# Kernel optimization log

Measured on AMD Instinct MI355X. Metric: run time of the kernel, lower is better.

## Reference

```python
import jax, jax.numpy as jnp
import numpy as np

B, N, NFEAT, NHID, NOUT, NMLP, NCLASS = 32, 1024, 128, 64, 64, 128, 2
ALPHA = 0.2  # leaky relu slope
NEG = -9e15


def setup_inputs() -> dict:
    key = jax.random.key(0)
    ks = jax.random.split(key, 12)
    x = jax.random.normal(ks[0], (B, N, NFEAT), dtype=jnp.float32)
    x_mask = (jax.random.uniform(ks[1], (B, N)) < 0.9).astype(jnp.float32)
    adj = (jax.random.uniform(ks[2], (B, N, N)) < 0.05).astype(jnp.float32)
    adj = jnp.maximum(adj, jnp.eye(N, dtype=jnp.float32)[None])  # self loops
    s = 0.02
    W0 = jax.random.normal(ks[3], (NFEAT, NHID), dtype=jnp.float32) * s
    a0 = jax.random.normal(ks[4], (2 * NHID, 1), dtype=jnp.float32) * s
    Wout = jax.random.normal(ks[5], (NHID, NOUT), dtype=jnp.float32) * s
    aout = jax.random.normal(ks[6], (2 * NOUT, 1), dtype=jnp.float32) * s
    W1 = jax.random.normal(ks[7], (NOUT, NMLP), dtype=jnp.float32) * s
    b1 = jnp.zeros((NMLP,), dtype=jnp.float32)
    W2 = jax.random.normal(ks[8], (NMLP, NCLASS), dtype=jnp.float32) * s
    b2 = jnp.zeros((NCLASS,), dtype=jnp.float32)
    return {"x": x, "x_mask": x_mask, "adj": adj, "W0": W0, "a0": a0,
            "Wout": Wout, "aout": aout, "W1": W1, "b1": b1, "W2": W2, "b2": b2}


def _gat_layer(h, adj, W, a):
    # h: [B,N,F_in], W: [F_in,F_out], a: [2*F_out,1]
    Wh = jnp.einsum('bnf,fh->bnh', h, W)                 # [B,N,F_out]
    d = W.shape[1]
    f1 = Wh @ a[:d]                                      # [B,N,1]
    f2 = Wh @ a[d:]                                      # [B,N,1]
    e = jax.nn.leaky_relu(f1 + jnp.swapaxes(f2, 1, 2), ALPHA)  # [B,N,N]
    e = jnp.where(adj > 0, e, NEG)
    attn = jax.nn.softmax(e, axis=-1)
    return jnp.einsum('bnm,bmh->bnh', attn, Wh)


def reference(x, x_mask, adj, W0, a0, Wout, aout, W1, b1, W2, b2):
    # Only head 0 reaches out_att in the original (zip truncation); dropout is
    # identity in eval mode.
    h = jax.nn.elu(_gat_layer(x, adj, W0, a0))           # concat=True -> elu
    h = jax.nn.elu(_gat_layer(h, adj, Wout, aout))       # F.elu applied outside
    m = x_mask[..., None]
    g = jnp.sum(h * m, axis=1) / jnp.maximum(jnp.sum(x_mask, axis=1, keepdims=True), 1.0)  # masked mean readout [B,NOUT]
    return jax.nn.relu(g @ W1 + b1) @ W2 + b2            # [B,NCLASS]
```

## Files before the change

### kernel.cpp

```cpp
#include <hip/hip_runtime.h>
#include <math.h>

#define BB 32
#define NN 1024
#define NFEAT 128
#define ALPHA 0.2f
#define MAXD 128

#define WH1_TILE_BLOCKS (BB * NN / 64)
#define ATTN_BLOCKS (BB * NN / 8)

template<int FIN>
__device__ __forceinline__ void wh_tile_body(
    const int blk, const int tid,
    const float* __restrict__ hin, const float* __restrict__ W,
    const float* __restrict__ a, float* __restrict__ Wh,
    float* __restrict__ f1, float* __restrict__ f2) {
  const int tx = tid & 15;
  const int ty = tid >> 4;
  const int row0 = blk * 64 + ty * 4;

  float4 acc[4];
#pragma unroll
  for (int i = 0; i < 4; ++i) acc[i] = make_float4(0.f, 0.f, 0.f, 0.f);

#pragma unroll 4
  for (int k = 0; k < FIN; k += 4) {
    float4 wv[4];
#pragma unroll
    for (int i = 0; i < 4; ++i)
      wv[i] = *reinterpret_cast<const float4*>(&W[(size_t)(k + i) * 64 + tx * 4]);
#pragma unroll
    for (int i = 0; i < 4; ++i) {
      const float4 xv = *reinterpret_cast<const float4*>(
          &hin[(size_t)(row0 + i) * FIN + k]);
      acc[i].x = fmaf(xv.x, wv[0].x, acc[i].x);
      acc[i].y = fmaf(xv.x, wv[0].y, acc[i].y);
      acc[i].z = fmaf(xv.x, wv[0].z, acc[i].z);
      acc[i].w = fmaf(xv.x, wv[0].w, acc[i].w);
      acc[i].x = fmaf(xv.y, wv[1].x, acc[i].x);
      acc[i].y = fmaf(xv.y, wv[1].y, acc[i].y);
      acc[i].z = fmaf(xv.y, wv[1].z, acc[i].z);
      acc[i].w = fmaf(xv.y, wv[1].w, acc[i].w);
      acc[i].x = fmaf(xv.z, wv[2].x, acc[i].x);
      acc[i].y = fmaf(xv.z, wv[2].y, acc[i].y);
      acc[i].z = fmaf(xv.z, wv[2].z, acc[i].z);
      acc[i].w = fmaf(xv.z, wv[2].w, acc[i].w);
      acc[i].x = fmaf(xv.w, wv[3].x, acc[i].x);
      acc[i].y = fmaf(xv.w, wv[3].y, acc[i].y);
      acc[i].z = fmaf(xv.w, wv[3].z, acc[i].z);
      acc[i].w = fmaf(xv.w, wv[3].w, acc[i].w);
    }
  }

  const float4 av1 = *reinterpret_cast<const float4*>(&a[tx * 4]);
  const float4 av2 = *reinterpret_cast<const float4*>(&a[64 + tx * 4]);
#pragma unroll
  for (int i = 0; i < 4; ++i) {
    const int row = row0 + i;
    *reinterpret_cast<float4*>(&Wh[(size_t)row * 64 + tx * 4]) = acc[i];
    float c1 = acc[i].x * av1.x + acc[i].y * av1.y + acc[i].z * av1.z + acc[i].w * av1.w;
    float c2 = acc[i].x * av2.x + acc[i].y * av2.y + acc[i].z * av2.z + acc[i].w * av2.w;
#pragma unroll
    for (int off = 8; off > 0; off >>= 1) {
      c1 += __shfl_xor(c1, off, 64);
      c2 += __shfl_xor(c2, off, 64);
    }
    if (tx == 0) { f1[row] = c1; f2[row] = c2; }
  }
}

__global__ __launch_bounds__(256) void wh1_kernel(
    const float* __restrict__ x, const float* __restrict__ W0,
    const float* __restrict__ a0, float* __restrict__ Wh,
    float* __restrict__ f1, float* __restrict__ f2) {
  wh_tile_body<NFEAT>(blockIdx.x, threadIdx.x, x, W0, a0, Wh, f1, f2);
}

__device__ __forceinline__ void gather2(
    const float* ps0, const unsigned short* ms0,
    const float* ps1, const unsigned short* ms1,
    const int bound, const float* __restrict__ Whb, const int lane,
    float& out0, float& out1) {
  float a0 = 0.f, a1 = 0.f, a2 = 0.f, a3 = 0.f;
  float b0 = 0.f, b1 = 0.f, b2 = 0.f, b3 = 0.f;
  for (int k = 0; k < bound; k += 4) {
    const float4  p0 = *reinterpret_cast<const float4*>(&ps0[k]);
    const ushort4 i0 = *reinterpret_cast<const ushort4*>(&ms0[k]);
    const float4  p1 = *reinterpret_cast<const float4*>(&ps1[k]);
    const ushort4 i1 = *reinterpret_cast<const ushort4*>(&ms1[k]);
    a0 = fmaf(p0.x, Whb[(size_t)i0.x * 64 + lane], a0);
    a1 = fmaf(p0.y, Whb[(size_t)i0.y * 64 + lane], a1);
    a2 = fmaf(p0.z, Whb[(size_t)i0.z * 64 + lane], a2);
    a3 = fmaf(p0.w, Whb[(size_t)i0.w * 64 + lane], a3);
    b0 = fmaf(p1.x, Whb[(size_t)i1.x * 64 + lane], b0);
    b1 = fmaf(p1.y, Whb[(size_t)i1.y * 64 + lane], b1);
    b2 = fmaf(p1.z, Whb[(size_t)i1.z * 64 + lane], b2);
    b3 = fmaf(p1.w, Whb[(size_t)i1.w * 64 + lane], b3);
  }
  out0 = (a0 + a1) + (a2 + a3);
  out1 = (b0 + b1) + (b2 + b3);
}

__global__ __launch_bounds__(256) void scan_attn1_kernel(
    const float* __restrict__ adj,
    const float* __restrict__ f1, const float* __restrict__ f2,
    const float* __restrict__ Wh,
    const float* __restrict__ Wnext, const float* __restrict__ anext,
    unsigned short* __restrict__ nbr, int* __restrict__ cnt,
    float* __restrict__ WhOut, float* __restrict__ f1o,
    float* __restrict__ f2o) {
  __shared__ float ps[4][2][MAXD];
  __shared__ unsigned short msh[4][2][MAXD];
  __shared__ float h1s[4][2][64];
  const int wv = threadIdx.x >> 6, lane = threadIdx.x & 63;
  const int j = blockIdx.x;
  const int batch = (j & 7) + 8 * (j >> 10);
  const int cp = (j >> 3) & 127;
  const int row0 = (batch * 256 + 2 * cp) * 4 + wv;

  float4 av[2][4];
#pragma unroll
  for (int rr = 0; rr < 2; ++rr)
#pragma unroll
    for (int c = 0; c < 4; ++c)
      av[rr][c] = *reinterpret_cast<const float4*>(
          &adj[(size_t)(row0 + rr * 4) * NN + c * 256 + lane * 4]);

#pragma unroll
  for (int rr = 0; rr < 2; ++rr) {
    msh[wv][rr][lane] = 0;
    msh[wv][rr][64 + lane] = 0;
  }

  const unsigned long long lmask = (1ull << lane) - 1ull;
  int count_r[2];
#pragma unroll
  for (int rr = 0; rr < 2; ++rr) {
    int count = 0;
#pragma unroll
    for (int c = 0; c < 4; ++c) {
      const int m = (av[rr][c].x > 0.f ? 1 : 0) | (av[rr][c].y > 0.f ? 2 : 0) |
                    (av[rr][c].z > 0.f ? 4 : 0) | (av[rr][c].w > 0.f ? 8 : 0);
      const unsigned long long b0 = __ballot(m & 1);
      const unsigned long long b1 = __ballot(m & 2);
      const unsigned long long b2 = __ballot(m & 4);
      const unsigned long long b3 = __ballot(m & 8);
      int base = count + __popcll(b0 & lmask) + __popcll(b1 & lmask) +
                 __popcll(b2 & lmask) + __popcll(b3 & lmask);
      const int e0 = c * 256 + lane * 4;
      if (m & 1) { if (base < MAXD) msh[wv][rr][base] = (unsigned short)(e0);     ++base; }
      if (m & 2) { if (base < MAXD) msh[wv][rr][base] = (unsigned short)(e0 + 1); ++base; }
      if (m & 4) { if (base < MAXD) msh[wv][rr][base] = (unsigned short)(e0 + 2); ++base; }
      if (m & 8) { if (base < MAXD) msh[wv][rr][base] = (unsigned short)(e0 + 3); ++base; }
      count += __popcll(b0) + __popcll(b1) + __popcll(b2) + __popcll(b3);
    }
    if (count > MAXD) count = MAXD;
    count_r[rr] = count;
    if (lane == 0) cnt[row0 + rr * 4] = count;
    const unsigned int lo = msh[wv][rr][2 * lane];
    const unsigned int hi = msh[wv][rr][2 * lane + 1];
    reinterpret_cast<unsigned int*>(nbr + (size_t)(row0 + rr * 4) * MAXD)[lane] =
        lo | (hi << 16);
  }

  const float* f2b = f2 + (size_t)batch * NN;
  const float f1v[2] = { f1[row0], f1[row0 + 4] };
#pragma unroll
  for (int rr = 0; rr < 2; ++rr) {
    const int cntr = count_r[rr];
    const int m0 = msh[wv][rr][lane];
    const int m1 = msh[wv][rr][64 + lane];
    const bool on0 = lane < cntr, on1 = 64 + lane < cntr;
    const float v0 = f1v[rr] + f2b[m0];
    const float v1 = f1v[rr] + f2b[m1];
    float e0v = on0 ? (v0 > 0.f ? v0 : ALPHA * v0) : -3e38f;
    float e1v = on1 ? (v1 > 0.f ? v1 : ALPHA * v1) : -3e38f;
    float lmax = fmaxf(e0v, e1v);
#pragma unroll
    for (int off = 32; off > 0; off >>= 1) lmax = fmaxf(lmax, __shfl_xor(lmax, off, 64));
    const float p0 = on0 ? __expf(e0v - lmax) : 0.f;
    const float p1 = on1 ? __expf(e1v - lmax) : 0.f;
    float ls = p0 + p1;
#pragma unroll
    for (int off = 32; off > 0; off >>= 1) ls += __shfl_xor(ls, off, 64);
    const float inv = 1.f / ls;
    ps[wv][rr][lane] = p0 * inv;
    ps[wv][rr][64 + lane] = p1 * inv;
  }

  const int cmax = count_r[0] > count_r[1] ? count_r[0] : count_r[1];
  const int bound = (cmax + 3) & ~3;
  const float* Whb = Wh + (size_t)batch * (NN * 64);
  float acc0, acc1;
  gather2(ps[wv][0], msh[wv][0], ps[wv][1], msh[wv][1], bound, Whb, lane,
          acc0, acc1);
  const float hv0 = acc0 > 0.f ? acc0 : expm1f(acc0);
  const float hv1 = acc1 > 0.f ? acc1 : expm1f(acc1);

  h1s[wv][0][lane] = hv0;
  h1s[wv][1][lane] = hv1;
  float s0 = 0.f, s1 = 0.f;
#pragma unroll 8
  for (int f = 0; f < 64; ++f) {
    const float w = Wnext[f * 64 + lane];
    s0 = fmaf(h1s[wv][0][f], w, s0);
    s1 = fmaf(h1s[wv][1][f], w, s1);
  }
  WhOut[(size_t)row0 * 64 + lane] = s0;
  WhOut[(size_t)(row0 + 4) * 64 + lane] = s1;
  const float a1v = anext[lane], a2v = anext[64 + lane];
  float c10 = s0 * a1v, c20 = s0 * a2v;
  float c11 = s1 * a1v, c21 = s1 * a2v;
#pragma unroll
  for (int off = 32; off > 0; off >>= 1) {
    c10 += __shfl_xor(c10, off, 64);
    c20 += __shfl_xor(c20, off, 64);
    c11 += __shfl_xor(c11, off, 64);
    c21 += __shfl_xor(c21, off, 64);
  }
  if (lane == 0) {
    f1o[row0] = c10;  f2o[row0] = c20;
    f1o[row0 + 4] = c11;  f2o[row0 + 4] = c21;
  }
}

__global__ __launch_bounds__(256) void attn2_kernel(
    const unsigned short* __restrict__ nbr, const int* __restrict__ cnt,
    const float* __restrict__ f1, const float* __restrict__ f2,
    const float* __restrict__ Wh, const float* __restrict__ mask,
    float* __restrict__ part2) {
  __shared__ float ps[4][2][MAXD];
  __shared__ unsigned short msh[4][2][MAXD];
  __shared__ float agg[4][2][64];
  const int wv = threadIdx.x >> 6, lane = threadIdx.x & 63;
  const int j = blockIdx.x;
  const int batch = (j & 7) + 8 * (j >> 10);
  const int cp = (j >> 3) & 127;
  const int row0 = (batch * 256 + 2 * cp) * 4 + wv;

  const float* f2b = f2 + (size_t)batch * NN;
  const float f1v[2] = { f1[row0], f1[row0 + 4] };
  int count_r[2];
#pragma unroll
  for (int rr = 0; rr < 2; ++rr) {
    int cntr = cnt[row0 + rr * 4];
    if (cntr > MAXD) cntr = MAXD;
    count_r[rr] = cntr;
    const unsigned short* nrow = nbr + (size_t)(row0 + rr * 4) * MAXD;
    const int m0 = nrow[lane];
    const int m1 = nrow[64 + lane];
    const bool on0 = lane < cntr, on1 = 64 + lane < cntr;
    const float v0 = f1v[rr] + f2b[m0];
    const float v1 = f1v[rr] + f2b[m1];
    float e0v = on0 ? (v0 > 0.f ? v0 : ALPHA * v0) : -3e38f;
    float e1v = on1 ? (v1 > 0.f ? v1 : ALPHA * v1) : -3e38f;
    float lmax = fmaxf(e0v, e1v);
#pragma unroll
    for (int off = 32; off > 0; off >>= 1) lmax = fmaxf(lmax, __shfl_xor(lmax, off, 64));
    const float p0 = on0 ? __expf(e0v - lmax) : 0.f;
    const float p1 = on1 ? __expf(e1v - lmax) : 0.f;
    float ls = p0 + p1;
#pragma unroll
    for (int off = 32; off > 0; off >>= 1) ls += __shfl_xor(ls, off, 64);
    const float inv = 1.f / ls;
    ps[wv][rr][lane] = p0 * inv;
    ps[wv][rr][64 + lane] = p1 * inv;
    msh[wv][rr][lane] = (unsigned short)(on0 ? m0 : 0);
    msh[wv][rr][64 + lane] = (unsigned short)(on1 ? m1 : 0);
  }

  const int cmax = count_r[0] > count_r[1] ? count_r[0] : count_r[1];
  const int bound = (cmax + 3) & ~3;
  const float* Whb = Wh + (size_t)batch * (NN * 64);
  float acc0, acc1;
  gather2(ps[wv][0], msh[wv][0], ps[wv][1], msh[wv][1], bound, Whb, lane,
          acc0, acc1);
  const float hv0 = acc0 > 0.f ? acc0 : expm1f(acc0);
  const float hv1 = acc1 > 0.f ? acc1 : expm1f(acc1);

  const float mv0 = mask[row0];
  const float mv1 = mask[row0 + 4];
  agg[wv][0][lane] = mv0 * hv0;
  agg[wv][1][lane] = mv1 * hv1;
  __syncthreads();
  if (wv < 2)
    part2[((size_t)batch * 256 + 2 * cp + wv) * 64 + lane] =
        (agg[0][wv][lane] + agg[1][wv][lane]) +
        (agg[2][wv][lane] + agg[3][wv][lane]);
}

__global__ __launch_bounds__(256) void mlp2_kernel(
    const float* __restrict__ part2, const float* __restrict__ mask,
    const float* __restrict__ W1, const float* __restrict__ b1,
    const float* __restrict__ W2, const float* __restrict__ b2,
    float* __restrict__ outp) {
  const int b = blockIdx.x;
  const int tid = threadIdx.x;
  const int wv = tid >> 6, lane = tid & 63;
  __shared__ float aggG[4][64];
  __shared__ float msW[4];
  __shared__ float g[64];
  __shared__ float hid[128];

  const float4 mv4 = *reinterpret_cast<const float4*>(&mask[(size_t)b * NN + tid * 4]);
  float ms = (mv4.x + mv4.y) + (mv4.z + mv4.w);
#pragma unroll
  for (int off = 32; off > 0; off >>= 1) ms += __shfl_xor(ms, off, 64);
  if (lane == 0) msW[wv] = ms;

  float gs = 0.f;
  const float* pb = part2 + ((size_t)b * 256 + wv * 64) * 64 + lane;
#pragma unroll 8
  for (int i = 0; i < 64; ++i) gs += pb[(size_t)i * 64];
  aggG[wv][lane] = gs;
  __syncthreads();
  const float denom = fmaxf((msW[0] + msW[1]) + (msW[2] + msW[3]), 1.0f);
  if (tid < 64)
    g[tid] = ((aggG[0][tid] + aggG[1][tid]) + (aggG[2][tid] + aggG[3][tid])) / denom;
  __syncthreads();
  if (tid < 128) {
    float s = b1[tid];
#pragma unroll 8
    for (int k = 0; k < 64; ++k) s += g[k] * W1[k * 128 + tid];
    hid[tid] = fmaxf(s, 0.f);
  }
  __syncthreads();
  if (tid < 2) {
    float o = b2[tid];
    for (int jj = 0; jj < 128; ++jj) o += hid[jj] * W2[jj * 2 + tid];
    outp[b * 2 + tid] = o;
  }
}

extern "C" void kernel_launch(void* const* d_in, const int* in_sizes, int n_in,
                              void* d_out, int out_size, void* d_ws, size_t ws_size,
                              hipStream_t stream) {
  const float* x      = (const float*)d_in[0];
  const float* x_mask = (const float*)d_in[1];
  const float* adj    = (const float*)d_in[2];
  const float* W0     = (const float*)d_in[3];
  const float* a0     = (const float*)d_in[4];
  const float* Wout   = (const float*)d_in[5];
  const float* aout   = (const float*)d_in[6];
  const float* W1     = (const float*)d_in[7];
  const float* b1     = (const float*)d_in[8];
  const float* W2     = (const float*)d_in[9];
  const float* b2     = (const float*)d_in[10];
  float* out = (float*)d_out;

  const int rows = BB * NN;

  float* ws = (float*)d_ws;
  float* Wh  = ws;
  float* Wh2 = Wh + (size_t)rows * 64;
  float* f1  = Wh2 + (size_t)rows * 64;
  float* f2  = f1 + rows;
  float* f1b = f2 + rows;
  float* f2b = f1b + rows;
  int*   cnt = (int*)(f2b + rows);
  unsigned short* nbr = (unsigned short*)(cnt + rows);
  float* part2 = (float*)(nbr + (size_t)rows * MAXD);

  wh1_kernel<<<WH1_TILE_BLOCKS, 256, 0, stream>>>(x, W0, a0, Wh, f1, f2);
  scan_attn1_kernel<<<ATTN_BLOCKS, 256, 0, stream>>>(
      adj, f1, f2, Wh, Wout, aout, nbr, cnt, Wh2, f1b, f2b);
  attn2_kernel<<<ATTN_BLOCKS, 256, 0, stream>>>(
      nbr, cnt, f1b, f2b, Wh2, x_mask, part2);
  mlp2_kernel<<<BB, 256, 0, stream>>>(part2, x_mask, W1, b1, W2, b2, out);
}
```

Before: 102.1 us.

## Process four rows per wave in scan_attn1 with software-prefetched adjacency rows

Restructures the first attention kernel so each wavefront handles four consecutive rows sequentially instead of two interleaved rows. The next row's adjacency is prefetched into registers while the current one is scanned, softmaxed and gathered. Neighbour byte offsets are precomputed in shared memory to simplify gather addressing, and the Wnext projection is amortized over four rows. Grid size halves and launch bounds request two blocks per CU, trading the two-row gather ILP and the batch-interleaved block mapping for serial per-row latency hidden by prefetch.

```diff
diff --git a/kernel.cpp b/kernel.cpp
--- a/kernel.cpp
+++ b/kernel.cpp
@@ -8,6 +8,7 @@
 #define MAXD 128
 
 #define WH1_TILE_BLOCKS (BB * NN / 64)
+#define SCAN_BLOCKS (BB * NN / 16)
 #define ATTN_BLOCKS (BB * NN / 8)
 
 template<int FIN>
@@ -75,6 +76,149 @@
     const float* __restrict__ a0, float* __restrict__ Wh,
     float* __restrict__ f1, float* __restrict__ f2) {
   wh_tile_body<NFEAT>(blockIdx.x, threadIdx.x, x, W0, a0, Wh, f1, f2);
+}
+
+__device__ __forceinline__ float ldw(const float* base, unsigned byte_off) {
+  return *reinterpret_cast<const float*>(
+      reinterpret_cast<const char*>(base) + byte_off);
+}
+
+__global__ __launch_bounds__(256, 2) void scan_attn1_kernel(
+    const float* __restrict__ adj,
+    const float* __restrict__ f1, const float* __restrict__ f2,
+    const float* __restrict__ Wh,
+    const float* __restrict__ Wnext, const float* __restrict__ anext,
+    unsigned short* __restrict__ nbr, int* __restrict__ cnt,
+    float* __restrict__ WhOut, float* __restrict__ f1o,
+    float* __restrict__ f2o) {
+  __shared__ __align__(16) float ps_s[4][MAXD];
+  __shared__ __align__(16) unsigned offs_s[4][MAXD];
+  __shared__ unsigned short msh_s[4][MAXD];
+  __shared__ float h1s_s[4][4][64];
+  const int wv = threadIdx.x >> 6, lane = threadIdx.x & 63;
+  const int lane4 = lane * 4;
+  const int row0 = blockIdx.x * 16 + wv * 4;
+  const int batch = row0 >> 10;
+  const float* f2b = f2 + (size_t)batch * NN;
+  const float* Whb = Wh + (size_t)batch * (NN * 64);
+  float* ps_w = ps_s[wv];
+  unsigned* offs_w = offs_s[wv];
+  unsigned short* msh_w = msh_s[wv];
+  const unsigned long long lmask = (1ull << lane) - 1ull;
+
+  float4 avA[4], avB[4];
+#pragma unroll
+  for (int c = 0; c < 4; ++c)
+    avA[c] = *reinterpret_cast<const float4*>(
+        &adj[(size_t)row0 * NN + c * 256 + lane4]);
+
+  auto body = [&](float4 (&cur)[4], float4 (&nxt)[4], const int i) {
+    const int row = row0 + i;
+    if (i < 3) {
+      const float* arow = adj + (size_t)(row + 1) * NN;
+#pragma unroll
+      for (int c = 0; c < 4; ++c)
+        nxt[c] = *reinterpret_cast<const float4*>(&arow[c * 256 + lane4]);
+    }
+    msh_w[lane] = 0;
+    msh_w[64 + lane] = 0;
+    int count = 0;
+#pragma unroll
+    for (int c = 0; c < 4; ++c) {
+      const int m = (cur[c].x > 0.f ? 1 : 0) | (cur[c].y > 0.f ? 2 : 0) |
+                    (cur[c].z > 0.f ? 4 : 0) | (cur[c].w > 0.f ? 8 : 0);
+      const unsigned long long b0 = __ballot(m & 1);
+      const unsigned long long b1 = __ballot(m & 2);
+      const unsigned long long b2 = __ballot(m & 4);
+      const unsigned long long b3 = __ballot(m & 8);
+      int base = count + __popcll(b0 & lmask) + __popcll(b1 & lmask) +
+                 __popcll(b2 & lmask) + __popcll(b3 & lmask);
+      const int e0 = c * 256 + lane4;
+      if (m & 1) { if (base < MAXD) msh_w[base] = (unsigned short)(e0);     ++base; }
+      if (m & 2) { if (base < MAXD) msh_w[base] = (unsigned short)(e0 + 1); ++base; }
+      if (m & 4) { if (base < MAXD) msh_w[base] = (unsigned short)(e0 + 2); ++base; }
+      if (m & 8) { if (base < MAXD) msh_w[base] = (unsigned short)(e0 + 3); ++base; }
+      count += __popcll(b0) + __popcll(b1) + __popcll(b2) + __popcll(b3);
+    }
+    if (count > MAXD) count = MAXD;
+    if (lane == 0) cnt[row] = count;
+    {
+      const unsigned lo = msh_w[2 * lane];
+      const unsigned hi = msh_w[2 * lane + 1];
+      reinterpret_cast<unsigned*>(nbr + (size_t)row * MAXD)[lane] =
+          lo | (hi << 16);
+    }
+    const int m0 = msh_w[lane];
+    const int m1 = msh_w[64 + lane];
+    offs_w[lane] = (unsigned)(m0 << 8);
+    offs_w[64 + lane] = (unsigned)(m1 << 8);
+    const float f1n = f1[row];
+    const bool on0 = lane < count, on1 = 64 + lane < count;
+    const float v0 = f1n + f2b[m0];
+    const float v1 = f1n + f2b[m1];
+    float e0v = on0 ? (v0 > 0.f ? v0 : ALPHA * v0) : -3e38f;
+    float e1v = on1 ? (v1 > 0.f ? v1 : ALPHA * v1) : -3e38f;
+    float lmax = fmaxf(e0v, e1v);
+#pragma unroll
+    for (int off = 32; off > 0; off >>= 1) lmax = fmaxf(lmax, __shfl_xor(lmax, off, 64));
+    const float p0 = on0 ? __expf(e0v - lmax) : 0.f;
+    const float p1 = on1 ? __expf(e1v - lmax) : 0.f;
+    float ls = p0 + p1;
+#pragma unroll
+    for (int off = 32; off > 0; off >>= 1) ls += __shfl_xor(ls, off, 64);
+    const float inv = 1.f / ls;
+    ps_w[lane] = p0 * inv;
+    ps_w[64 + lane] = p1 * inv;
+    const int bound = (count + 3) & ~3;
+    float a0 = 0.f, a1 = 0.f, a2 = 0.f, a3 = 0.f;
+    for (int k = 0; k < bound; k += 4) {
+      const float4 p = *reinterpret_cast<const float4*>(&ps_w[k]);
+      const uint4  o = *reinterpret_cast<const uint4*>(&offs_w[k]);
+      a0 = fmaf(p.x, ldw(Whb, o.x + lane4), a0);
+      a1 = fmaf(p.y, ldw(Whb, o.y + lane4), a1);
+      a2 = fmaf(p.z, ldw(Whb, o.z + lane4), a2);
+      a3 = fmaf(p.w, ldw(Whb, o.w + lane4), a3);
+    }
+    const float acc = (a0 + a1) + (a2 + a3);
+    h1s_s[wv][i][lane] = acc > 0.f ? acc : expm1f(acc);
+  };
+
+  body(avA, avB, 0);
+  body(avB, avA, 1);
+  body(avA, avB, 2);
+  body(avB, avA, 3);
+
+  float s0 = 0.f, s1 = 0.f, s2 = 0.f, s3 = 0.f;
+#pragma unroll 8
+  for (int f = 0; f < 64; ++f) {
+    const float w = Wnext[f * 64 + lane];
+    s0 = fmaf(h1s_s[wv][0][f], w, s0);
+    s1 = fmaf(h1s_s[wv][1][f], w, s1);
+    s2 = fmaf(h1s_s[wv][2][f], w, s2);
+    s3 = fmaf(h1s_s[wv][3][f], w, s3);
+  }
+  WhOut[(size_t)(row0 + 0) * 64 + lane] = s0;
+  WhOut[(size_t)(row0 + 1) * 64 + lane] = s1;
+  WhOut[(size_t)(row0 + 2) * 64 + lane] = s2;
+  WhOut[(size_t)(row0 + 3) * 64 + lane] = s3;
+  const float a1v = anext[lane], a2v = anext[64 + lane];
+  float c1r[4] = { s0 * a1v, s1 * a1v, s2 * a1v, s3 * a1v };
+  float c2r[4] = { s0 * a2v, s1 * a2v, s2 * a2v, s3 * a2v };
+#pragma unroll
+  for (int off = 32; off > 0; off >>= 1) {
+#pragma unroll
+    for (int i = 0; i < 4; ++i) {
+      c1r[i] += __shfl_xor(c1r[i], off, 64);
+      c2r[i] += __shfl_xor(c2r[i], off, 64);
+    }
+  }
+  if (lane == 0) {
+#pragma unroll
+    for (int i = 0; i < 4; ++i) {
+      f1o[row0 + i] = c1r[i];
+      f2o[row0 + i] = c2r[i];
+    }
+  }
 }
 
 __device__ __forceinline__ void gather2(
@@ -102,129 +246,6 @@
   out1 = (b0 + b1) + (b2 + b3);
 }
 
-__global__ __launch_bounds__(256) void scan_attn1_kernel(
-    const float* __restrict__ adj,
-    const float* __restrict__ f1, const float* __restrict__ f2,
-    const float* __restrict__ Wh,
-    const float* __restrict__ Wnext, const float* __restrict__ anext,
-    unsigned short* __restrict__ nbr, int* __restrict__ cnt,
-    float* __restrict__ WhOut, float* __restrict__ f1o,
-    float* __restrict__ f2o) {
-  __shared__ float ps[4][2][MAXD];
-  __shared__ unsigned short msh[4][2][MAXD];
-  __shared__ float h1s[4][2][64];
-  const int wv = threadIdx.x >> 6, lane = threadIdx.x & 63;
-  const int j = blockIdx.x;
-  const int batch = (j & 7) + 8 * (j >> 10);
-  const int cp = (j >> 3) & 127;
-  const int row0 = (batch * 256 + 2 * cp) * 4 + wv;
-
-  float4 av[2][4];
-#pragma unroll
-  for (int rr = 0; rr < 2; ++rr)
-#pragma unroll
-    for (int c = 0; c < 4; ++c)
-      av[rr][c] = *reinterpret_cast<const float4*>(
-          &adj[(size_t)(row0 + rr * 4) * NN + c * 256 + lane * 4]);
-
-#pragma unroll
-  for (int rr = 0; rr < 2; ++rr) {
-    msh[wv][rr][lane] = 0;
-    msh[wv][rr][64 + lane] = 0;
-  }
-
-  const unsigned long long lmask = (1ull << lane) - 1ull;
-  int count_r[2];
-#pragma unroll
-  for (int rr = 0; rr < 2; ++rr) {
-    int count = 0;
-#pragma unroll
-    for (int c = 0; c < 4; ++c) {
-      const int m = (av[rr][c].x > 0.f ? 1 : 0) | (av[rr][c].y > 0.f ? 2 : 0) |
-                    (av[rr][c].z > 0.f ? 4 : 0) | (av[rr][c].w > 0.f ? 8 : 0);
-      const unsigned long long b0 = __ballot(m & 1);
-      const unsigned long long b1 = __ballot(m & 2);
-      const unsigned long long b2 = __ballot(m & 4);
-      const unsigned long long b3 = __ballot(m & 8);
-      int base = count + __popcll(b0 & lmask) + __popcll(b1 & lmask) +
-                 __popcll(b2 & lmask) + __popcll(b3 & lmask);
-      const int e0 = c * 256 + lane * 4;
-      if (m & 1) { if (base < MAXD) msh[wv][rr][base] = (unsigned short)(e0);     ++base; }
-      if (m & 2) { if (base < MAXD) msh[wv][rr][base] = (unsigned short)(e0 + 1); ++base; }
-      if (m & 4) { if (base < MAXD) msh[wv][rr][base] = (unsigned short)(e0 + 2); ++base; }
-      if (m & 8) { if (base < MAXD) msh[wv][rr][base] = (unsigned short)(e0 + 3); ++base; }
-      count += __popcll(b0) + __popcll(b1) + __popcll(b2) + __popcll(b3);
-    }
-    if (count > MAXD) count = MAXD;
-    count_r[rr] = count;
-    if (lane == 0) cnt[row0 + rr * 4] = count;
-    const unsigned int lo = msh[wv][rr][2 * lane];
-    const unsigned int hi = msh[wv][rr][2 * lane + 1];
-    reinterpret_cast<unsigned int*>(nbr + (size_t)(row0 + rr * 4) * MAXD)[lane] =
-        lo | (hi << 16);
-  }
-
-  const float* f2b = f2 + (size_t)batch * NN;
-  const float f1v[2] = { f1[row0], f1[row0 + 4] };
-#pragma unroll
-  for (int rr = 0; rr < 2; ++rr) {
-    const int cntr = count_r[rr];
-    const int m0 = msh[wv][rr][lane];
-    const int m1 = msh[wv][rr][64 + lane];
-    const bool on0 = lane < cntr, on1 = 64 + lane < cntr;
-    const float v0 = f1v[rr] + f2b[m0];
-    const float v1 = f1v[rr] + f2b[m1];
-    float e0v = on0 ? (v0 > 0.f ? v0 : ALPHA * v0) : -3e38f;
-    float e1v = on1 ? (v1 > 0.f ? v1 : ALPHA * v1) : -3e38f;
-    float lmax = fmaxf(e0v, e1v);
-#pragma unroll
-    for (int off = 32; off > 0; off >>= 1) lmax = fmaxf(lmax, __shfl_xor(lmax, off, 64));
-    const float p0 = on0 ? __expf(e0v - lmax) : 0.f;
-    const float p1 = on1 ? __expf(e1v - lmax) : 0.f;
-    float ls = p0 + p1;
-#pragma unroll
-    for (int off = 32; off > 0; off >>= 1) ls += __shfl_xor(ls, off, 64);
-    const float inv = 1.f / ls;
-    ps[wv][rr][lane] = p0 * inv;
-    ps[wv][rr][64 + lane] = p1 * inv;
-  }
-
-  const int cmax = count_r[0] > count_r[1] ? count_r[0] : count_r[1];
-  const int bound = (cmax + 3) & ~3;
-  const float* Whb = Wh + (size_t)batch * (NN * 64);
-  float acc0, acc1;
-  gather2(ps[wv][0], msh[wv][0], ps[wv][1], msh[wv][1], bound, Whb, lane,
-          acc0, acc1);
-  const float hv0 = acc0 > 0.f ? acc0 : expm1f(acc0);
-  const float hv1 = acc1 > 0.f ? acc1 : expm1f(acc1);
-
-  h1s[wv][0][lane] = hv0;
-  h1s[wv][1][lane] = hv1;
-  float s0 = 0.f, s1 = 0.f;
-#pragma unroll 8
-  for (int f = 0; f < 64; ++f) {
-    const float w = Wnext[f * 64 + lane];
-    s0 = fmaf(h1s[wv][0][f], w, s0);
-    s1 = fmaf(h1s[wv][1][f], w, s1);
-  }
-  WhOut[(size_t)row0 * 64 + lane] = s0;
-  WhOut[(size_t)(row0 + 4) * 64 + lane] = s1;
-  const float a1v = anext[lane], a2v = anext[64 + lane];
-  float c10 = s0 * a1v, c20 = s0 * a2v;
-  float c11 = s1 * a1v, c21 = s1 * a2v;
-#pragma unroll
-  for (int off = 32; off > 0; off >>= 1) {
-    c10 += __shfl_xor(c10, off, 64);
-    c20 += __shfl_xor(c20, off, 64);
-    c11 += __shfl_xor(c11, off, 64);
-    c21 += __shfl_xor(c21, off, 64);
-  }
-  if (lane == 0) {
-    f1o[row0] = c10;  f2o[row0] = c20;
-    f1o[row0 + 4] = c11;  f2o[row0 + 4] = c21;
-  }
-}
-
 __global__ __launch_bounds__(256) void attn2_kernel(
     const unsigned short* __restrict__ nbr, const int* __restrict__ cnt,
     const float* __restrict__ f1, const float* __restrict__ f2,
@@ -363,7 +384,7 @@
   float* part2 = (float*)(nbr + (size_t)rows * MAXD);
 
   wh1_kernel<<<WH1_TILE_BLOCKS, 256, 0, stream>>>(x, W0, a0, Wh, f1, f2);
-  scan_attn1_kernel<<<ATTN_BLOCKS, 256, 0, stream>>>(
+  scan_attn1_kernel<<<SCAN_BLOCKS, 256, 0, stream>>>(
       adj, f1, f2, Wh, Wout, aout, nbr, cnt, Wh2, f1b, f2b);
   attn2_kernel<<<ATTN_BLOCKS, 256, 0, stream>>>(
       nbr, cnt, f1b, f2b, Wh2, x_mask, part2);
```

New measurement: 127.7 us. 25.1% more time.

## Gather neighbour rows as float4 across four slots and issue adj loads via asm

Applied to the files above, without the earlier changes.

The neighbour gather in both attention kernels now has each lane load a float4 of 4 features for one of 4 neighbours at a time, instead of one scalar per lane per neighbour. Partial sums are then reduced across the 4 slots with cross-lane shuffles. This cuts the number of load instructions and widens each memory transaction, at the cost of extra shuffle reductions. The adjacency row loads in scan_attn1 are also issued through inline global_load_dwordx4 with an explicit waitcnt and sched barrier, so they are in flight while shared memory is being cleared.

```diff
diff --git a/kernel.cpp b/kernel.cpp
--- a/kernel.cpp
+++ b/kernel.cpp
@@ -9,6 +9,10 @@
 
 #define WH1_TILE_BLOCKS (BB * NN / 64)
 #define ATTN_BLOCKS (BB * NN / 8)
+
+__device__ __forceinline__ void gld_f4(float4& d, const float* a) {
+  asm volatile("global_load_dwordx4 %0, %1, off" : "=v"(d) : "v"(a));
+}
 
 template<int FIN>
 __device__ __forceinline__ void wh_tile_body(
@@ -77,29 +81,50 @@
   wh_tile_body<NFEAT>(blockIdx.x, threadIdx.x, x, W0, a0, Wh, f1, f2);
 }
 
-__device__ __forceinline__ void gather2(
+__device__ __forceinline__ void gather4(
     const float* ps0, const unsigned short* ms0,
     const float* ps1, const unsigned short* ms1,
-    const int bound, const float* __restrict__ Whb, const int lane,
-    float& out0, float& out1) {
-  float a0 = 0.f, a1 = 0.f, a2 = 0.f, a3 = 0.f;
-  float b0 = 0.f, b1 = 0.f, b2 = 0.f, b3 = 0.f;
+    const int bound, const float* __restrict__ Whb,
+    const int slot, const int fq, float4& outA, float4& outB) {
+  float4 accA = make_float4(0.f, 0.f, 0.f, 0.f);
+  float4 accB = make_float4(0.f, 0.f, 0.f, 0.f);
+  const float* WhF = Whb + fq * 4;
   for (int k = 0; k < bound; k += 4) {
-    const float4  p0 = *reinterpret_cast<const float4*>(&ps0[k]);
-    const ushort4 i0 = *reinterpret_cast<const ushort4*>(&ms0[k]);
-    const float4  p1 = *reinterpret_cast<const float4*>(&ps1[k]);
-    const ushort4 i1 = *reinterpret_cast<const ushort4*>(&ms1[k]);
-    a0 = fmaf(p0.x, Whb[(size_t)i0.x * 64 + lane], a0);
-    a1 = fmaf(p0.y, Whb[(size_t)i0.y * 64 + lane], a1);
-    a2 = fmaf(p0.z, Whb[(size_t)i0.z * 64 + lane], a2);
-    a3 = fmaf(p0.w, Whb[(size_t)i0.w * 64 + lane], a3);
-    b0 = fmaf(p1.x, Whb[(size_t)i1.x * 64 + lane], b0);
-    b1 = fmaf(p1.y, Whb[(size_t)i1.y * 64 + lane], b1);
-    b2 = fmaf(p1.z, Whb[(size_t)i1.z * 64 + lane], b2);
-    b3 = fmaf(p1.w, Whb[(size_t)i1.w * 64 + lane], b3);
-  }
-  out0 = (a0 + a1) + (a2 + a3);
-  out1 = (b0 + b1) + (b2 + b3);
+    const int ia = ms0[k + slot];
+    const int ib = ms1[k + slot];
+    const float pa = ps0[k + slot];
+    const float pb = ps1[k + slot];
+    const float4 wa = *reinterpret_cast<const float4*>(&WhF[(size_t)ia * 64]);
+    const float4 wb = *reinterpret_cast<const float4*>(&WhF[(size_t)ib * 64]);
+    accA.x = fmaf(pa, wa.x, accA.x);
+    accA.y = fmaf(pa, wa.y, accA.y);
+    accA.z = fmaf(pa, wa.z, accA.z);
+    accA.w = fmaf(pa, wa.w, accA.w);
+    accB.x = fmaf(pb, wb.x, accB.x);
+    accB.y = fmaf(pb, wb.y, accB.y);
+    accB.z = fmaf(pb, wb.z, accB.z);
+    accB.w = fmaf(pb, wb.w, accB.w);
+  }
+#pragma unroll
+  for (int off = 16; off <= 32; off <<= 1) {
+    accA.x += __shfl_xor(accA.x, off, 64);
+    accA.y += __shfl_xor(accA.y, off, 64);
+    accA.z += __shfl_xor(accA.z, off, 64);
+    accA.w += __shfl_xor(accA.w, off, 64);
+    accB.x += __shfl_xor(accB.x, off, 64);
+    accB.y += __shfl_xor(accB.y, off, 64);
+    accB.z += __shfl_xor(accB.z, off, 64);
+    accB.w += __shfl_xor(accB.w, off, 64);
+  }
+  outA = accA;
+  outB = accB;
+}
+
+__device__ __forceinline__ float4 elu4(const float4 v) {
+  return make_float4(v.x > 0.f ? v.x : expm1f(v.x),
+                     v.y > 0.f ? v.y : expm1f(v.y),
+                     v.z > 0.f ? v.z : expm1f(v.z),
+                     v.w > 0.f ? v.w : expm1f(v.w));
 }
 
 __global__ __launch_bounds__(256) void scan_attn1_kernel(
@@ -110,38 +135,43 @@
     unsigned short* __restrict__ nbr, int* __restrict__ cnt,
     float* __restrict__ WhOut, float* __restrict__ f1o,
     float* __restrict__ f2o) {
-  __shared__ float ps[4][2][MAXD];
-  __shared__ unsigned short msh[4][2][MAXD];
-  __shared__ float h1s[4][2][64];
+  __shared__ __align__(16) float ps[4][2][MAXD];
+  __shared__ __align__(16) unsigned short msh[4][2][MAXD];
+  __shared__ __align__(16) float h1s[4][2][64];
   const int wv = threadIdx.x >> 6, lane = threadIdx.x & 63;
+  const int slot = lane >> 4, fq = lane & 15;
   const int j = blockIdx.x;
   const int batch = (j & 7) + 8 * (j >> 10);
   const int cp = (j >> 3) & 127;
   const int row0 = (batch * 256 + 2 * cp) * 4 + wv;
 
-  float4 av[2][4];
-#pragma unroll
-  for (int rr = 0; rr < 2; ++rr)
-#pragma unroll
-    for (int c = 0; c < 4; ++c)
-      av[rr][c] = *reinterpret_cast<const float4*>(
-          &adj[(size_t)(row0 + rr * 4) * NN + c * 256 + lane * 4]);
-
-#pragma unroll
-  for (int rr = 0; rr < 2; ++rr) {
-    msh[wv][rr][lane] = 0;
-    msh[wv][rr][64 + lane] = 0;
-  }
+  const float f1v0 = f1[row0];
+  const float f1v1 = f1[row0 + 4];
+  const float* f2b = f2 + (size_t)batch * NN;
+
+  const float* ar0 = adj + (size_t)row0 * NN + lane * 4;
+  const float* ar1 = adj + (size_t)(row0 + 4) * NN + lane * 4;
+  float4 av00, av01, av02, av03, av10, av11, av12, av13;
+  gld_f4(av00, ar0);        gld_f4(av01, ar0 + 256);
+  gld_f4(av02, ar0 + 512);  gld_f4(av03, ar0 + 768);
+  gld_f4(av10, ar1);        gld_f4(av11, ar1 + 256);
+  gld_f4(av12, ar1 + 512);  gld_f4(av13, ar1 + 768);
+
+  msh[wv][0][lane] = 0;  msh[wv][0][64 + lane] = 0;
+  msh[wv][1][lane] = 0;  msh[wv][1][64 + lane] = 0;
+
+  asm volatile("s_waitcnt vmcnt(0)" ::: "memory");
+  __builtin_amdgcn_sched_barrier(0);
 
   const unsigned long long lmask = (1ull << lane) - 1ull;
-  int count_r[2];
-#pragma unroll
-  for (int rr = 0; rr < 2; ++rr) {
+  auto compact = [&](const float4& c0, const float4& c1, const float4& c2,
+                     const float4& c3, unsigned short* mrow) -> int {
     int count = 0;
 #pragma unroll
     for (int c = 0; c < 4; ++c) {
-      const int m = (av[rr][c].x > 0.f ? 1 : 0) | (av[rr][c].y > 0.f ? 2 : 0) |
-                    (av[rr][c].z > 0.f ? 4 : 0) | (av[rr][c].w > 0.f ? 8 : 0);
+      const float4& cv = (c == 0) ? c0 : (c == 1) ? c1 : (c == 2) ? c2 : c3;
+      const int m = (cv.x > 0.f ? 1 : 0) | (cv.y > 0.f ? 2 : 0) |
+                    (cv.z > 0.f ? 4 : 0) | (cv.w > 0.f ? 8 : 0);
       const unsigned long long b0 = __ballot(m & 1);
       const unsigned long long b1 = __ballot(m & 2);
       const unsigned long long b2 = __ballot(m & 4);
@@ -149,31 +179,35 @@
       int base = count + __popcll(b0 & lmask) + __popcll(b1 & lmask) +
                  __popcll(b2 & lmask) + __popcll(b3 & lmask);
       const int e0 = c * 256 + lane * 4;
-      if (m & 1) { if (base < MAXD) msh[wv][rr][base] = (unsigned short)(e0);     ++base; }
-      if (m & 2) { if (base < MAXD) msh[wv][rr][base] = (unsigned short)(e0 + 1); ++base; }
-      if (m & 4) { if (base < MAXD) msh[wv][rr][base] = (unsigned short)(e0 + 2); ++base; }
-      if (m & 8) { if (base < MAXD) msh[wv][rr][base] = (unsigned short)(e0 + 3); ++base; }
+      if (m & 1) { if (base < MAXD) mrow[base] = (unsigned short)(e0);     ++base; }
+      if (m & 2) { if (base < MAXD) mrow[base] = (unsigned short)(e0 + 1); ++base; }
+      if (m & 4) { if (base < MAXD) mrow[base] = (unsigned short)(e0 + 2); ++base; }
+      if (m & 8) { if (base < MAXD) mrow[base] = (unsigned short)(e0 + 3); ++base; }
       count += __popcll(b0) + __popcll(b1) + __popcll(b2) + __popcll(b3);
     }
-    if (count > MAXD) count = MAXD;
-    count_r[rr] = count;
-    if (lane == 0) cnt[row0 + rr * 4] = count;
-    const unsigned int lo = msh[wv][rr][2 * lane];
-    const unsigned int hi = msh[wv][rr][2 * lane + 1];
-    reinterpret_cast<unsigned int*>(nbr + (size_t)(row0 + rr * 4) * MAXD)[lane] =
-        lo | (hi << 16);
-  }
-
-  const float* f2b = f2 + (size_t)batch * NN;
-  const float f1v[2] = { f1[row0], f1[row0 + 4] };
+    return count < MAXD ? count : MAXD;
+  };
+  const int count0 = compact(av00, av01, av02, av03, msh[wv][0]);
+  const int count1 = compact(av10, av11, av12, av13, msh[wv][1]);
+  if (lane == 0) { cnt[row0] = count0; cnt[row0 + 4] = count1; }
+  {
+    const unsigned lo0 = msh[wv][0][2 * lane];
+    const unsigned hi0 = msh[wv][0][2 * lane + 1];
+    reinterpret_cast<unsigned*>(nbr + (size_t)row0 * MAXD)[lane] = lo0 | (hi0 << 16);
+    const unsigned lo1 = msh[wv][1][2 * lane];
+    const unsigned hi1 = msh[wv][1][2 * lane + 1];
+    reinterpret_cast<unsigned*>(nbr + (size_t)(row0 + 4) * MAXD)[lane] = lo1 | (hi1 << 16);
+  }
+
 #pragma unroll
   for (int rr = 0; rr < 2; ++rr) {
-    const int cntr = count_r[rr];
+    const int cntr = rr == 0 ? count0 : count1;
+    const float f1n = rr == 0 ? f1v0 : f1v1;
     const int m0 = msh[wv][rr][lane];
     const int m1 = msh[wv][rr][64 + lane];
     const bool on0 = lane < cntr, on1 = 64 + lane < cntr;
-    const float v0 = f1v[rr] + f2b[m0];
-    const float v1 = f1v[rr] + f2b[m1];
+    const float v0 = f1n + f2b[m0];
+    const float v1 = f1n + f2b[m1];
     float e0v = on0 ? (v0 > 0.f ? v0 : ALPHA * v0) : -3e38f;
     float e1v = on1 ? (v1 > 0.f ? v1 : ALPHA * v1) : -3e38f;
     float lmax = fmaxf(e0v, e1v);
@@ -189,17 +223,17 @@
     ps[wv][rr][64 + lane] = p1 * inv;
   }
 
-  const int cmax = count_r[0] > count_r[1] ? count_r[0] : count_r[1];
+  const int cmax = count0 > count1 ? count0 : count1;
   const int bound = (cmax + 3) & ~3;
   const float* Whb = Wh + (size_t)batch * (NN * 64);
-  float acc0, acc1;
-  gather2(ps[wv][0], msh[wv][0], ps[wv][1], msh[wv][1], bound, Whb, lane,
-          acc0, acc1);
-  const float hv0 = acc0 > 0.f ? acc0 : expm1f(acc0);
-  const float hv1 = acc1 > 0.f ? acc1 : expm1f(acc1);
-
-  h1s[wv][0][lane] = hv0;
-  h1s[wv][1][lane] = hv1;
+  float4 accA, accB;
+  gather4(ps[wv][0], msh[wv][0], ps[wv][1], msh[wv][1], bound, Whb,
+          slot, fq, accA, accB);
+  if (slot == 0) {
+    *reinterpret_cast<float4*>(&h1s[wv][0][fq * 4]) = elu4(accA);
+    *reinterpret_cast<float4*>(&h1s[wv][1][fq * 4]) = elu4(accB);
+  }
+
   float s0 = 0.f, s1 = 0.f;
 #pragma unroll 8
   for (int f = 0; f < 64; ++f) {
@@ -230,10 +264,11 @@
     const float* __restrict__ f1, const float* __restrict__ f2,
     const float* __restrict__ Wh, const float* __restrict__ mask,
     float* __restrict__ part2) {
-  __shared__ float ps[4][2][MAXD];
-  __shared__ unsigned short msh[4][2][MAXD];
-  __shared__ float agg[4][2][64];
+  __shared__ __align__(16) float ps[4][2][MAXD];
+  __shared__ __align__(16) unsigned short msh[4][2][MAXD];
+  __shared__ __align__(16) float agg[4][2][64];
   const int wv = threadIdx.x >> 6, lane = threadIdx.x & 63;
+  const int slot = lane >> 4, fq = lane & 15;
   const int j = blockIdx.x;
   const int batch = (j & 7) + 8 * (j >> 10);
   const int cp = (j >> 3) & 127;
@@ -273,16 +308,19 @@
   const int cmax = count_r[0] > count_r[1] ? count_r[0] : count_r[1];
   const int bound = (cmax + 3) & ~3;
   const float* Whb = Wh + (size_t)batch * (NN * 64);
-  float acc0, acc1;
-  gather2(ps[wv][0], msh[wv][0], ps[wv][1], msh[wv][1], bound, Whb, lane,
-          acc0, acc1);
-  const float hv0 = acc0 > 0.f ? acc0 : expm1f(acc0);
-  const float hv1 = acc1 > 0.f ? acc1 : expm1f(acc1);
-
+  float4 accA, accB;
+  gather4(ps[wv][0], msh[wv][0], ps[wv][1], msh[wv][1], bound, Whb,
+          slot, fq, accA, accB);
   const float mv0 = mask[row0];
   const float mv1 = mask[row0 + 4];
-  agg[wv][0][lane] = mv0 * hv0;
-  agg[wv][1][lane] = mv1 * hv1;
+  if (slot == 0) {
+    const float4 h0 = elu4(accA);
+    const float4 h1 = elu4(accB);
+    *reinterpret_cast<float4*>(&agg[wv][0][fq * 4]) =
+        make_float4(mv0 * h0.x, mv0 * h0.y, mv0 * h0.z, mv0 * h0.w);
+    *reinterpret_cast<float4*>(&agg[wv][1][fq * 4]) =
+        make_float4(mv1 * h1.x, mv1 * h1.y, mv1 * h1.z, mv1 * h1.w);
+  }
   __syncthreads();
   if (wv < 2)
     part2[((size_t)batch * 256 + 2 * cp + wv) * 64 + lane] =
```

Result: no change. 101.8 us (-0.2%).
